# Optimization experiments

Measured on AMD Instinct MI355X. Metric: run time of the kernel, lower is better.

The kernel has to match this reference:

```python
import jax, jax.numpy as jnp
import numpy as np

B, S, E, H = 2, 512, 1024, 16
D = E // H  # 64


def setup_inputs() -> dict:
    key = jax.random.key(0)
    ks = jax.random.split(key, 8)
    q = jax.random.normal(ks[0], (B, S, E), dtype=jnp.float32)
    k = jax.random.normal(ks[1], (B, S, E), dtype=jnp.float32)
    v = jax.random.normal(ks[2], (B, S, E), dtype=jnp.float32)
    # per-position bilinear term, scaled down so scores stay in a sane range
    p = jax.random.normal(ks[3], (B, S, H, D, D), dtype=jnp.float32) * 0.05
    # causal additive mask [S, S]
    neg = jnp.float32(-1e9)
    mask = jnp.where(jnp.triu(jnp.ones((S, S), dtype=bool), k=1), neg, jnp.float32(0.0))
    scale = 1.0 / np.sqrt(E)
    Wq = jax.random.normal(ks[4], (E, E), dtype=jnp.float32) * scale
    Wk = jax.random.normal(ks[5], (E, E), dtype=jnp.float32) * scale
    Wv = jax.random.normal(ks[6], (E, E), dtype=jnp.float32) * scale
    Wo = jax.random.normal(ks[7], (E, E), dtype=jnp.float32) * scale
    return {"q": q, "k": k, "v": v, "p": p, "mask": mask,
            "Wq": Wq, "Wk": Wk, "Wv": Wv, "Wo": Wo}


def reference(q, k, v, p, mask, Wq, Wk, Wv, Wo):
    b, s, e = q.shape
    h, d = p.shape[2], p.shape[3]
    # projections (torch Linear: y = x @ W.T), split into heads -> [b,h,s,d]
    qh = (q @ Wq.T).reshape(b, s, h, d).transpose(0, 2, 1, 3)
    kh = (k @ Wk.T).reshape(b, -1, h, d).transpose(0, 2, 1, 3)
    vh = (v @ Wv.T).reshape(b, -1, h, d).transpose(0, 2, 1, 3)
    # scores = einsum('bhse,bshef,bhtf->bhst') done in two steps
    qp = jnp.einsum('bhse,bshef->bhsf', qh, p)          # [b,h,s,d]
    scores = jnp.einsum('bhsf,bhtf->bhst', qp, kh)      # [b,h,s,t]
    scores = scores / jnp.sqrt(jnp.float32(d))
    scores = scores + mask[None, None, :, :]
    w = jax.nn.softmax(scores, axis=-1)
    att = jnp.einsum('bhst,bhtd->bshd', w, vh).reshape(b, s, e)
    return att @ Wo.T
```

## Files before the change

### kernel.cpp

```cpp
#include <hip/hip_runtime.h>
#include <hip/hip_bf16.h>

namespace {

constexpr int kB = 2, kS = 512, kE = 1024, kH = 16, kD = 64;
constexpr int kM = kB * kS;
constexpr int kBH = kB * kH;
constexpr int kSP = 524;

typedef short bf16x8 __attribute__((ext_vector_type(8)));
typedef float f32x4 __attribute__((ext_vector_type(4)));

__device__ __forceinline__ unsigned short f2bf(float f) {
  __hip_bfloat16 h = __float2bfloat16(f);
  unsigned short u;
  __builtin_memcpy(&u, &h, 2);
  return u;
}
__device__ __forceinline__ float bf2f(unsigned short u) {
  unsigned int x = (unsigned int)u << 16;
  float f;
  __builtin_memcpy(&f, &x, 4);
  return f;
}

__global__ void cvt7_kernel(const float* __restrict__ s0, const float* __restrict__ s1,
                            const float* __restrict__ s2, const float* __restrict__ s3,
                            const float* __restrict__ s4, const float* __restrict__ s5,
                            const float* __restrict__ s6,
                            unsigned short* __restrict__ dstBase) {
  const float* srcs[7] = {s0, s1, s2, s3, s4, s5, s6};
  const float* src = srcs[blockIdx.y];
  unsigned short* dst = dstBase + (size_t)blockIdx.y * (kM * kE);
  int i = (blockIdx.x * blockDim.x + threadIdx.x) * 4;
  float4 v = *reinterpret_cast<const float4*>(src + i);
  ushort4 o;
  o.x = f2bf(v.x); o.y = f2bf(v.y); o.z = f2bf(v.z); o.w = f2bf(v.w);
  *reinterpret_cast<ushort4*>(dst + i) = o;
}

__device__ __forceinline__ void mfma_tile_32x32(
    const unsigned short* __restrict__ A, int lda,
    const unsigned short* __restrict__ Bm, int ldb,
    int row0, int col0, int K, f32x4 acc[2][2]) {
  const int lane = threadIdx.x & 63;
  const int r = lane & 15;
  const int ko = (lane >> 4) * 8;
  const unsigned short* a0 = A + (size_t)(row0 + r) * lda + ko;
  const unsigned short* a1 = a0 + 16 * (size_t)lda;
  const unsigned short* b0 = Bm + (size_t)(col0 + r) * ldb + ko;
  const unsigned short* b1 = b0 + 16 * (size_t)ldb;
  for (int kk = 0; kk < K; kk += 32) {
    bf16x8 af0 = *reinterpret_cast<const bf16x8*>(a0 + kk);
    bf16x8 af1 = *reinterpret_cast<const bf16x8*>(a1 + kk);
    bf16x8 bg0 = *reinterpret_cast<const bf16x8*>(b0 + kk);
    bf16x8 bg1 = *reinterpret_cast<const bf16x8*>(b1 + kk);
    acc[0][0] = __builtin_amdgcn_mfma_f32_16x16x32_bf16(af0, bg0, acc[0][0], 0, 0, 0);
    acc[0][1] = __builtin_amdgcn_mfma_f32_16x16x32_bf16(af0, bg1, acc[0][1], 0, 0, 0);
    acc[1][0] = __builtin_amdgcn_mfma_f32_16x16x32_bf16(af1, bg0, acc[1][0], 0, 0, 0);
    acc[1][1] = __builtin_amdgcn_mfma_f32_16x16x32_bf16(af1, bg1, acc[1][1], 0, 0, 0);
  }
}

__global__ __launch_bounds__(256) void proj_q_kernel(
    const unsigned short* __restrict__ qb, const unsigned short* __restrict__ Wq,
    unsigned short* __restrict__ qh) {
  const int w = threadIdx.x >> 6;
  const int row0 = blockIdx.y * 64 + (w >> 1) * 32;
  const int col0 = blockIdx.x * 64 + (w & 1) * 32;
  f32x4 acc[2][2] = {};
  mfma_tile_32x32(qb, kE, Wq, kE, row0, col0, kE, acc);
  const int lane = threadIdx.x & 63;
#pragma unroll
  for (int ri = 0; ri < 2; ++ri)
#pragma unroll
    for (int ci = 0; ci < 2; ++ci)
#pragma unroll
      for (int r = 0; r < 4; ++r) {
        int i = row0 + 16 * ri + 4 * (lane >> 4) + r;
        int j = col0 + 16 * ci + (lane & 15);
        int b = i >> 9, s = i & 511, h = j >> 6, d = j & 63;
        qh[(((size_t)(b * kH + h) * kS) + s) * kD + d] = f2bf(acc[ri][ci][r]);
      }
}

__global__ __launch_bounds__(256) void mega_kernel(
    const float* __restrict__ p, const unsigned short* __restrict__ qh,
    unsigned short* __restrict__ qp,
    const unsigned short* __restrict__ kb, const unsigned short* __restrict__ vb,
    const unsigned short* __restrict__ Wk, const unsigned short* __restrict__ Wv,
    unsigned short* __restrict__ kh, unsigned short* __restrict__ vhT) {
  __shared__ float qsh[kH][kD];
  const int flat = blockIdx.x;
  const int mod = flat % 3;
  if (mod == 2) {
    const int pidx = flat / 3;
    const int which = pidx >> 8;
    const int tile = pidx & 255;
    const int w = threadIdx.x >> 6;
    const int row0 = (tile >> 4) * 64 + (w >> 1) * 32;
    const int col0 = (tile & 15) * 64 + (w & 1) * 32;
    const unsigned short* A = which ? vb : kb;
    const unsigned short* W = which ? Wv : Wk;
    f32x4 acc[2][2] = {};
    mfma_tile_32x32(A, kE, W, kE, row0, col0, kE, acc);
    const int lane = threadIdx.x & 63;
#pragma unroll
    for (int ri = 0; ri < 2; ++ri)
#pragma unroll
      for (int ci = 0; ci < 2; ++ci)
#pragma unroll
        for (int r = 0; r < 4; ++r) {
          int i = row0 + 16 * ri + 4 * (lane >> 4) + r;
          int j = col0 + 16 * ci + (lane & 15);
          int b = i >> 9, s = i & 511, h = j >> 6, d = j & 63;
          unsigned short val = f2bf(acc[ri][ci][r]);
          if (which)
            vhT[(((size_t)(b * kH + h) * kD) + d) * kS + s] = val;
          else
            kh[(((size_t)(b * kH + h) * kS) + s) * kD + d] = val;
        }
  } else {
    const int bs = (flat / 3) * 2 + mod;
    const int b = bs >> 9, s = bs & 511;
    const int t = threadIdx.x;
    {
      int h = t >> 4, d4 = (t & 15) * 4;
      const unsigned short* qr =
          qh + (((size_t)(b * kH + h) * kS) + s) * kD + d4;
      ushort4 u = *reinterpret_cast<const ushort4*>(qr);
      qsh[h][d4 + 0] = bf2f(u.x);
      qsh[h][d4 + 1] = bf2f(u.y);
      qsh[h][d4 + 2] = bf2f(u.z);
      qsh[h][d4 + 3] = bf2f(u.w);
    }
    __syncthreads();
    const int w = t >> 6;
    const int lane = t & 63;
    const int g = lane >> 4, fi = lane & 15;
#pragma unroll
    for (int j = 0; j < 4; ++j) {
      const int hh = w * 4 + j;
      const f32x4* p4 = reinterpret_cast<const f32x4*>(p) +
                        ((size_t)(bs * kH + hh) << 10);
      f32x4 acc = {0.f, 0.f, 0.f, 0.f};
#pragma unroll
      for (int iter = 0; iter < 16; ++iter) {
        f32x4 pv = p4[iter * 64 + lane];
        float qv = qsh[hh][iter * 4 + g];
        acc[0] += qv * pv[0];
        acc[1] += qv * pv[1];
        acc[2] += qv * pv[2];
        acc[3] += qv * pv[3];
      }
#pragma unroll
      for (int m = 16; m <= 32; m <<= 1) {
        acc[0] += __shfl_xor(acc[0], m);
        acc[1] += __shfl_xor(acc[1], m);
        acc[2] += __shfl_xor(acc[2], m);
        acc[3] += __shfl_xor(acc[3], m);
      }
      if (g == 0) {
        ushort4 o;
        o.x = f2bf(acc[0]); o.y = f2bf(acc[1]);
        o.z = f2bf(acc[2]); o.w = f2bf(acc[3]);
        *reinterpret_cast<ushort4*>(
            qp + (((size_t)(b * kH + hh) * kS) + s) * kD + fi * 4) = o;
      }
    }
  }
}

__global__ __launch_bounds__(256) void attn_kernel(
    const unsigned short* __restrict__ qp,
    const unsigned short* __restrict__ kh,
    const unsigned short* __restrict__ vhT,
    unsigned short* __restrict__ att) {
  __shared__ float S[32 * kSP];
  const int bh = blockIdx.y;
  const int b = bh >> 4, h = bh & 15;
  const int bx = blockIdx.x;
  const int row0 = bx * 32;
  const int ncol = row0 + 32;
  const int w = threadIdx.x >> 6;
  const int lane = threadIdx.x & 63;
  const int g = lane >> 4, c = lane & 15;

  const unsigned short* Abase = qp + (size_t)bh * kS * kD;
  const unsigned short* Kbase = kh + (size_t)bh * kS * kD;

  bf16x8 qa[2][2];
#pragma unroll
  for (int ri = 0; ri < 2; ++ri)
#pragma unroll
    for (int kk = 0; kk < 2; ++kk)
      qa[ri][kk] = *reinterpret_cast<const bf16x8*>(
          Abase + (size_t)(row0 + 16 * ri + c) * kD + kk * 32 + g * 8);

  for (int ct = w; ct <= bx; ct += 4) {
    const int col0 = ct * 32;
    const unsigned short* kr0 = Kbase + (size_t)(col0 + c) * kD + g * 8;
    bf16x8 kb00 = *reinterpret_cast<const bf16x8*>(kr0);
    bf16x8 kb01 = *reinterpret_cast<const bf16x8*>(kr0 + 32);
    bf16x8 kb10 = *reinterpret_cast<const bf16x8*>(kr0 + 16 * kD);
    bf16x8 kb11 = *reinterpret_cast<const bf16x8*>(kr0 + 16 * kD + 32);
    f32x4 sacc[2][2] = {};
    sacc[0][0] = __builtin_amdgcn_mfma_f32_16x16x32_bf16(qa[0][0], kb00, sacc[0][0], 0, 0, 0);
    sacc[0][0] = __builtin_amdgcn_mfma_f32_16x16x32_bf16(qa[0][1], kb01, sacc[0][0], 0, 0, 0);
    sacc[0][1] = __builtin_amdgcn_mfma_f32_16x16x32_bf16(qa[0][0], kb10, sacc[0][1], 0, 0, 0);
    sacc[0][1] = __builtin_amdgcn_mfma_f32_16x16x32_bf16(qa[0][1], kb11, sacc[0][1], 0, 0, 0);
    sacc[1][0] = __builtin_amdgcn_mfma_f32_16x16x32_bf16(qa[1][0], kb00, sacc[1][0], 0, 0, 0);
    sacc[1][0] = __builtin_amdgcn_mfma_f32_16x16x32_bf16(qa[1][1], kb01, sacc[1][0], 0, 0, 0);
    sacc[1][1] = __builtin_amdgcn_mfma_f32_16x16x32_bf16(qa[1][0], kb10, sacc[1][1], 0, 0, 0);
    sacc[1][1] = __builtin_amdgcn_mfma_f32_16x16x32_bf16(qa[1][1], kb11, sacc[1][1], 0, 0, 0);
#pragma unroll
    for (int ri = 0; ri < 2; ++ri)
#pragma unroll
      for (int ci = 0; ci < 2; ++ci)
#pragma unroll
        for (int r = 0; r < 4; ++r) {
          int il = 16 * ri + 4 * g + r;
          int jg = col0 + 16 * ci + c;
          float val = sacc[ri][ci][r] * 0.125f;
          if (jg > row0 + il) val = -1e9f;
          S[il * kSP + jg] = val;
        }
  }
  __syncthreads();

#pragma unroll
  for (int rr = 0; rr < 8; ++rr) {
    const int i = w * 8 + rr;
    float v[8];
    float m = -1e30f;
#pragma unroll
    for (int ii = 0; ii < 8; ++ii) {
      int j = lane + 64 * ii;
      v[ii] = (j < ncol) ? S[i * kSP + j] : -1e30f;
      m = fmaxf(m, v[ii]);
    }
#pragma unroll
    for (int off = 32; off; off >>= 1) m = fmaxf(m, __shfl_xor(m, off));
    float e[8], sum = 0.f;
#pragma unroll
    for (int ii = 0; ii < 8; ++ii) {
      e[ii] = __expf(v[ii] - m);
      sum += e[ii];
    }
#pragma unroll
    for (int off = 32; off; off >>= 1) sum += __shfl_xor(sum, off);
    const float inv = 1.0f / sum;
#pragma unroll
    for (int ii = 0; ii < 8; ++ii) S[i * kSP + lane + 64 * ii] = e[ii] * inv;
  }
  __syncthreads();

  const int d0 = w * 16;
  const unsigned short* Vbase = vhT + (size_t)(bh * kD + d0 + c) * kS;
  f32x4 oacc[2] = {};
  const int nk = bx + 1;
  for (int ks = 0; ks < nk; ++ks) {
    const int kb = ks * 32;
    bf16x8 vfrag = *reinterpret_cast<const bf16x8*>(Vbase + kb + g * 8);
#pragma unroll
    for (int ri = 0; ri < 2; ++ri) {
      const float* sp = &S[(16 * ri + c) * kSP + kb + g * 8];
      float4 x0 = *reinterpret_cast<const float4*>(sp);
      float4 x1 = *reinterpret_cast<const float4*>(sp + 4);
      bf16x8 pa;
      pa[0] = (short)f2bf(x0.x); pa[1] = (short)f2bf(x0.y);
      pa[2] = (short)f2bf(x0.z); pa[3] = (short)f2bf(x0.w);
      pa[4] = (short)f2bf(x1.x); pa[5] = (short)f2bf(x1.y);
      pa[6] = (short)f2bf(x1.z); pa[7] = (short)f2bf(x1.w);
      oacc[ri] = __builtin_amdgcn_mfma_f32_16x16x32_bf16(pa, vfrag, oacc[ri], 0, 0, 0);
    }
  }
#pragma unroll
  for (int ri = 0; ri < 2; ++ri)
#pragma unroll
    for (int r = 0; r < 4; ++r) {
      int s = row0 + 16 * ri + 4 * g + r;
      int d = d0 + c;
      att[((size_t)(b * kS + s) * kE) + h * kD + d] = f2bf(oacc[ri][r]);
    }
}

__global__ __launch_bounds__(256) void out_kernel(
    const unsigned short* __restrict__ att, const unsigned short* __restrict__ Wo,
    float* __restrict__ out) {
  const int w = threadIdx.x >> 6;
  const int row0 = blockIdx.y * 64 + (w >> 1) * 32;
  const int col0 = blockIdx.x * 64 + (w & 1) * 32;
  f32x4 acc[2][2] = {};
  mfma_tile_32x32(att, kE, Wo, kE, row0, col0, kE, acc);
  const int lane = threadIdx.x & 63;
#pragma unroll
  for (int ri = 0; ri < 2; ++ri)
#pragma unroll
    for (int ci = 0; ci < 2; ++ci)
#pragma unroll
      for (int r = 0; r < 4; ++r) {
        int i = row0 + 16 * ri + 4 * (lane >> 4) + r;
        int j = col0 + 16 * ci + (lane & 15);
        out[(size_t)i * kE + j] = acc[ri][ci][r];
      }
}

}

extern "C" void kernel_launch(void* const* d_in, const int* in_sizes, int n_in,
                              void* d_out, int out_size, void* d_ws,
                              size_t ws_size, hipStream_t stream) {
  const float* q = (const float*)d_in[0];
  const float* k = (const float*)d_in[1];
  const float* v = (const float*)d_in[2];
  const float* p = (const float*)d_in[3];
  const float* Wq = (const float*)d_in[5];
  const float* Wk = (const float*)d_in[6];
  const float* Wv = (const float*)d_in[7];
  const float* Wo = (const float*)d_in[8];
  float* out = (float*)d_out;

  char* ws = (char*)d_ws;
  size_t off = 0;
  auto alloc = [&](size_t bytes) {
    void* ptr = ws + off;
    off += (bytes + 255) & ~(size_t)255;
    return ptr;
  };
  const size_t nME = (size_t)kM * kE;
  unsigned short* qb = (unsigned short*)alloc(nME * 2);
  unsigned short* kb = (unsigned short*)alloc(nME * 2);
  unsigned short* vb = (unsigned short*)alloc(nME * 2);
  unsigned short* Wqb = (unsigned short*)alloc(nME * 2);
  unsigned short* Wkb = (unsigned short*)alloc(nME * 2);
  unsigned short* Wvb = (unsigned short*)alloc(nME * 2);
  unsigned short* Wob = (unsigned short*)alloc(nME * 2);
  unsigned short* qhB = (unsigned short*)alloc(nME * 2);
  unsigned short* khB = (unsigned short*)alloc(nME * 2);
  unsigned short* vhTB = (unsigned short*)alloc(nME * 2);
  unsigned short* qpB = (unsigned short*)alloc(nME * 2);
  unsigned short* attB = (unsigned short*)alloc(nME * 2);

  cvt7_kernel<<<dim3(kM * kE / (256 * 4), 7), 256, 0, stream>>>(
      q, k, v, Wq, Wk, Wv, Wo, qb);

  proj_q_kernel<<<dim3(kE / 64, kM / 64), 256, 0, stream>>>(qb, Wqb, qhB);

  mega_kernel<<<1536, 256, 0, stream>>>(p, qhB, qpB, kb, vb, Wkb, Wvb, khB,
                                        vhTB);

  attn_kernel<<<dim3(kS / 32, kBH), 256, 0, stream>>>(qpB, khB, vhTB, attB);

  out_kernel<<<dim3(kE / 64, kM / 64), 256, 0, stream>>>(attB, Wob, out);
}
```

Baseline: 144.7 us.

## Fuse Q projection with fp32 inputs into conversion kernel, drop separate launch

The separate fp32-to-bf16 conversion kernel and Q projection kernel are merged into one launch. The first 256 blocks compute the Q projection straight from fp32 q and Wq, converting fragments in registers. The remaining blocks convert k, v, Wk, Wv and Wo to bf16 as before. This removes one kernel launch and the bf16 round trip for q and Wq, and lets the projection overlap with the conversion. In exchange, the projection blocks read twice as many bytes per fragment and do the conversion arithmetic inside the GEMM loop.

```diff
diff --git a/kernel.cpp b/kernel.cpp
--- a/kernel.cpp
+++ b/kernel.cpp
@@ -23,20 +23,16 @@
   __builtin_memcpy(&f, &x, 4);
   return f;
 }
-
-__global__ void cvt7_kernel(const float* __restrict__ s0, const float* __restrict__ s1,
-                            const float* __restrict__ s2, const float* __restrict__ s3,
-                            const float* __restrict__ s4, const float* __restrict__ s5,
-                            const float* __restrict__ s6,
-                            unsigned short* __restrict__ dstBase) {
-  const float* srcs[7] = {s0, s1, s2, s3, s4, s5, s6};
-  const float* src = srcs[blockIdx.y];
-  unsigned short* dst = dstBase + (size_t)blockIdx.y * (kM * kE);
-  int i = (blockIdx.x * blockDim.x + threadIdx.x) * 4;
-  float4 v = *reinterpret_cast<const float4*>(src + i);
-  ushort4 o;
-  o.x = f2bf(v.x); o.y = f2bf(v.y); o.z = f2bf(v.z); o.w = f2bf(v.w);
-  *reinterpret_cast<ushort4*>(dst + i) = o;
+__device__ __forceinline__ bf16x8 f32frag(const float* __restrict__ ptr) {
+  f32x4 a = *reinterpret_cast<const f32x4*>(ptr);
+  f32x4 b = *reinterpret_cast<const f32x4*>(ptr + 4);
+  bf16x8 r;
+#pragma unroll
+  for (int i = 0; i < 4; ++i) {
+    r[i] = (short)f2bf(a[i]);
+    r[4 + i] = (short)f2bf(b[i]);
+  }
+  return r;
 }
 
 __device__ __forceinline__ void mfma_tile_32x32(
@@ -62,26 +58,66 @@
   }
 }
 
-__global__ __launch_bounds__(256) void proj_q_kernel(
-    const unsigned short* __restrict__ qb, const unsigned short* __restrict__ Wq,
+__device__ __forceinline__ void mfma_tile_32x32_f32(
+    const float* __restrict__ A, int lda, const float* __restrict__ Bm,
+    int ldb, int row0, int col0, int K, f32x4 acc[2][2]) {
+  const int lane = threadIdx.x & 63;
+  const int r = lane & 15;
+  const int ko = (lane >> 4) * 8;
+  const float* a0 = A + (size_t)(row0 + r) * lda + ko;
+  const float* a1 = a0 + 16 * (size_t)lda;
+  const float* b0 = Bm + (size_t)(col0 + r) * ldb + ko;
+  const float* b1 = b0 + 16 * (size_t)ldb;
+  for (int kk = 0; kk < K; kk += 32) {
+    bf16x8 af0 = f32frag(a0 + kk);
+    bf16x8 af1 = f32frag(a1 + kk);
+    bf16x8 bg0 = f32frag(b0 + kk);
+    bf16x8 bg1 = f32frag(b1 + kk);
+    acc[0][0] = __builtin_amdgcn_mfma_f32_16x16x32_bf16(af0, bg0, acc[0][0], 0, 0, 0);
+    acc[0][1] = __builtin_amdgcn_mfma_f32_16x16x32_bf16(af0, bg1, acc[0][1], 0, 0, 0);
+    acc[1][0] = __builtin_amdgcn_mfma_f32_16x16x32_bf16(af1, bg0, acc[1][0], 0, 0, 0);
+    acc[1][1] = __builtin_amdgcn_mfma_f32_16x16x32_bf16(af1, bg1, acc[1][1], 0, 0, 0);
+  }
+}
+
+__global__ __launch_bounds__(256) void head_kernel(
+    const float* __restrict__ q, const float* __restrict__ Wq,
+    const float* __restrict__ k, const float* __restrict__ v,
+    const float* __restrict__ Wk, const float* __restrict__ Wv,
+    const float* __restrict__ Wo, unsigned short* __restrict__ cvt5,
     unsigned short* __restrict__ qh) {
-  const int w = threadIdx.x >> 6;
-  const int row0 = blockIdx.y * 64 + (w >> 1) * 32;
-  const int col0 = blockIdx.x * 64 + (w & 1) * 32;
-  f32x4 acc[2][2] = {};
-  mfma_tile_32x32(qb, kE, Wq, kE, row0, col0, kE, acc);
-  const int lane = threadIdx.x & 63;
-#pragma unroll
-  for (int ri = 0; ri < 2; ++ri)
-#pragma unroll
-    for (int ci = 0; ci < 2; ++ci)
-#pragma unroll
-      for (int r = 0; r < 4; ++r) {
-        int i = row0 + 16 * ri + 4 * (lane >> 4) + r;
-        int j = col0 + 16 * ci + (lane & 15);
-        int b = i >> 9, s = i & 511, h = j >> 6, d = j & 63;
-        qh[(((size_t)(b * kH + h) * kS) + s) * kD + d] = f2bf(acc[ri][ci][r]);
-      }
+  const int bid = blockIdx.x;
+  if (bid < 256) {
+    const int w = threadIdx.x >> 6;
+    const int row0 = (bid >> 4) * 64 + (w >> 1) * 32;
+    const int col0 = (bid & 15) * 64 + (w & 1) * 32;
+    f32x4 acc[2][2] = {};
+    mfma_tile_32x32_f32(q, kE, Wq, kE, row0, col0, kE, acc);
+    const int lane = threadIdx.x & 63;
+#pragma unroll
+    for (int ri = 0; ri < 2; ++ri)
+#pragma unroll
+      for (int ci = 0; ci < 2; ++ci)
+#pragma unroll
+        for (int r = 0; r < 4; ++r) {
+          int i = row0 + 16 * ri + 4 * (lane >> 4) + r;
+          int j = col0 + 16 * ci + (lane & 15);
+          int b = i >> 9, s = i & 511, h = j >> 6, d = j & 63;
+          qh[(((size_t)(b * kH + h) * kS) + s) * kD + d] = f2bf(acc[ri][ci][r]);
+        }
+  } else {
+    const int cb = bid - 256;
+    const int tt = cb >> 10;
+    const int c = cb & 1023;
+    const float* srcs[5] = {k, v, Wk, Wv, Wo};
+    const float* src = srcs[tt];
+    unsigned short* dst = cvt5 + (size_t)tt * (kM * kE);
+    int i = (c * 256 + threadIdx.x) * 4;
+    float4 v4 = *reinterpret_cast<const float4*>(src + i);
+    ushort4 o;
+    o.x = f2bf(v4.x); o.y = f2bf(v4.y); o.z = f2bf(v4.z); o.w = f2bf(v4.w);
+    *reinterpret_cast<ushort4*>(dst + i) = o;
+  }
 }
 
 __global__ __launch_bounds__(256) void mega_kernel(
@@ -329,23 +365,21 @@
     return ptr;
   };
   const size_t nME = (size_t)kM * kE;
-  unsigned short* qb = (unsigned short*)alloc(nME * 2);
-  unsigned short* kb = (unsigned short*)alloc(nME * 2);
-  unsigned short* vb = (unsigned short*)alloc(nME * 2);
-  unsigned short* Wqb = (unsigned short*)alloc(nME * 2);
-  unsigned short* Wkb = (unsigned short*)alloc(nME * 2);
-  unsigned short* Wvb = (unsigned short*)alloc(nME * 2);
-  unsigned short* Wob = (unsigned short*)alloc(nME * 2);
+  unsigned short* cvt5 = (unsigned short*)alloc(nME * 2 * 5);
   unsigned short* qhB = (unsigned short*)alloc(nME * 2);
   unsigned short* khB = (unsigned short*)alloc(nME * 2);
   unsigned short* vhTB = (unsigned short*)alloc(nME * 2);
   unsigned short* qpB = (unsigned short*)alloc(nME * 2);
   unsigned short* attB = (unsigned short*)alloc(nME * 2);
 
-  cvt7_kernel<<<dim3(kM * kE / (256 * 4), 7), 256, 0, stream>>>(
-      q, k, v, Wq, Wk, Wv, Wo, qb);
-
-  proj_q_kernel<<<dim3(kE / 64, kM / 64), 256, 0, stream>>>(qb, Wqb, qhB);
+  unsigned short* kb = cvt5;
+  unsigned short* vb = cvt5 + nME;
+  unsigned short* Wkb = cvt5 + 2 * nME;
+  unsigned short* Wvb = cvt5 + 3 * nME;
+  unsigned short* Wob = cvt5 + 4 * nME;
+
+  head_kernel<<<256 + 5 * 1024, 256, 0, stream>>>(q, Wq, k, v, Wk, Wv, Wo,
+                                                  cvt5, qhB);
 
   mega_kernel<<<1536, 256, 0, stream>>>(p, qhB, qpB, kb, vb, Wkb, Wvb, khB,
                                         vhTB);
```

After: 151.2 us. 1.05x slower.
